# Performance work log

Measured on AMD Instinct MI355X. Metric: run time of the kernel, lower is better.

The kernel has to match this reference:

```python
import jax, jax.numpy as jnp
import numpy as np

B, H, S, D = 4, 16, 4096, 64

def setup_inputs() -> dict:
    key = jax.random.key(0)
    kq, kk, kv, km = jax.random.split(key, 4)
    Q = jax.random.normal(kq, (B, H, S, D), dtype=jnp.float32)
    K = jax.random.normal(kk, (B, H, S, D), dtype=jnp.float32)
    V = jax.random.normal(kv, (B, H, S, D), dtype=jnp.float32)
    mask = jax.random.randint(km, (B, S), 0, 2, dtype=jnp.int32)
    return {"Q": Q, "K": K, "V": V, "mask": mask}

def reference(Q, K, V, mask):
    Q = jax.nn.relu(Q)
    K = jax.nn.relu(K)
    # zero out masked-out key positions: mask [B,S] -> [B,1,S,1]
    m = mask.astype(bool)[:, None, :, None]
    K = jnp.where(m, K, jnp.zeros((), K.dtype))
    # attn_inter = K^T V : [B,H,D,D]
    attn_inter = jnp.einsum('bhsd,bhse->bhde', K, V)
    # attn_weights = Q @ attn_inter : [B,H,S,D]
    attn_weights = jnp.einsum('bhsd,bhde->bhse', Q, attn_inter)
    # norm = Q @ sum_s K : [B,H,S,1]
    k_sum = K.sum(axis=2)  # [B,H,D]
    norm = jnp.einsum('bhsd,bhd->bhs', Q, k_sum)[..., None]
    return attn_weights / norm
```

## Files before the change

### kernel.cpp

```cpp
#include <hip/hip_runtime.h>
#include <hip/hip_bf16.h>

#define SDIM 4096
#define DDIM 64
#define HN   16
#define BH   64
#define NC   16

typedef __attribute__((ext_vector_type(8))) short short8;
typedef __attribute__((ext_vector_type(4))) float f32x4;

static __device__ __forceinline__ short f2bfs(float f) {
    __hip_bfloat16 h = __float2bfloat16(f);
    return *reinterpret_cast<short*>(&h);
}

__global__ __launch_bounds__(256, 4) void k1_kv(
    const float* __restrict__ K, const float* __restrict__ V,
    const int* __restrict__ mask,
    float* __restrict__ KVp, float* __restrict__ ksump)
{
    __shared__ float kb[4096];
    const int tid = threadIdx.x;
    const int w = tid >> 6, l = tid & 63;
    const int a = l & 15, q = l >> 4;
    const int bh = blockIdx.x >> 4, ch = blockIdx.x & 15;
    const int b  = bh >> 4;
    const long base = (long)bh * SDIM * DDIM;
    const int s0 = ch * 256;

    f32x4 acc[4];
#pragma unroll
    for (int i = 0; i < 4; ++i) acc[i] = (f32x4){0.f, 0.f, 0.f, 0.f};
    float ksacc[4] = {0.f, 0.f, 0.f, 0.f};

    for (int st = 0; st < 8; ++st) {
        const int sb = st * 32;
        const float* kp = K + base + (long)(s0 + sb + q * 8) * DDIM + a;
        const float* vp = V + base + (long)(s0 + sb + q * 8) * DDIM + w * 16 + a;
        const int*   mp = mask + b * SDIM + s0 + sb + q * 8;

        float kf[4][8], vf[8];
        int   mi[8];
#pragma unroll
        for (int j = 0; j < 8; ++j) {
            mi[j] = mp[j];
#pragma unroll
            for (int dt = 0; dt < 4; ++dt)
                kf[dt][j] = kp[j * 64 + dt * 16];
            vf[j] = vp[j * 64];
        }

        short8 af[4], bf;
#pragma unroll
        for (int dt = 0; dt < 4; ++dt) {
            short8 ta;
#pragma unroll
            for (int j = 0; j < 8; ++j) {
                float x = fmaxf(kf[dt][j], 0.f);
                x = mi[j] ? x : 0.f;
                ksacc[dt] += x;
                ta[j] = f2bfs(x);
            }
            af[dt] = ta;
        }
#pragma unroll
        for (int j = 0; j < 8; ++j) bf[j] = f2bfs(vf[j]);

#pragma unroll
        for (int dt = 0; dt < 4; ++dt)
            acc[dt] = __builtin_amdgcn_mfma_f32_16x16x32_bf16(
                af[dt], bf, acc[dt], 0, 0, 0);
    }

#pragma unroll
    for (int dt = 0; dt < 4; ++dt) {
        ksacc[dt] += __shfl_xor(ksacc[dt], 16);
        ksacc[dt] += __shfl_xor(ksacc[dt], 32);
    }
    if (w == 0 && q == 0) {
#pragma unroll
        for (int dt = 0; dt < 4; ++dt)
            ksump[((long)bh * NC + ch) * 64 + dt * 16 + a] = ksacc[dt];
    }

    __syncthreads();
#pragma unroll
    for (int dt = 0; dt < 4; ++dt)
#pragma unroll
        for (int r = 0; r < 4; ++r) {
            const int d = dt * 16 + q * 4 + r;
            const int e = w * 16 + a;
            kb[d * 64 + (e ^ (((d >> 3) & 3) << 4))] = acc[dt][r];
        }
    __syncthreads();
    float* outp = KVp + ((long)bh * NC + ch) * 4096;
#pragma unroll
    for (int i = 0; i < 16; ++i) {
        const int idx = i * 256 + tid;
        const int d = idx >> 6, e = idx & 63;
        outp[idx] = kb[d * 64 + (e ^ (((d >> 3) & 3) << 4))];
    }
}

__global__ __launch_bounds__(256) void k2_reduce(
    const float* __restrict__ KVp, const float* __restrict__ ksump,
    float* __restrict__ KV, float* __restrict__ ksum)
{
    const int bh = blockIdx.x >> 2;
    const int qt = blockIdx.x & 3;
    const int tid = threadIdx.x;
#pragma unroll
    for (int i = 0; i < 4; ++i) {
        const int idx = qt * 1024 + i * 256 + tid;
        float v = 0.f;
#pragma unroll
        for (int c = 0; c < NC; ++c) v += KVp[((long)bh * NC + c) * 4096 + idx];
        KV[(long)bh * 4096 + idx] = v;
    }
    if (qt == 0 && tid < 64) {
        float v = 0.f;
#pragma unroll
        for (int c = 0; c < NC; ++c) v += ksump[((long)bh * NC + c) * 64 + tid];
        ksum[bh * 64 + tid] = v;
    }
}

__global__ __launch_bounds__(256, 4) void k3_out(
    const float* __restrict__ Q, const float* __restrict__ KVm,
    const float* __restrict__ ksum, float* __restrict__ out)
{
    __shared__ float cbuf[4][16 * 68];
    const int tid  = threadIdx.x;
    const int w    = tid >> 6;
    const int l    = tid & 63;
    const int r16  = l & 15;
    const int quad = l >> 4;
    const int bh    = blockIdx.x >> 4;
    const int strip = blockIdx.x & 15;

    const float* kvp = KVm + (long)bh * 4096;
    short8 bfrag[2][4];
#pragma unroll
    for (int kh = 0; kh < 2; ++kh)
#pragma unroll
        for (int n = 0; n < 4; ++n) {
            short8 tmp;
#pragma unroll
            for (int j = 0; j < 8; ++j)
                tmp[j] = f2bfs(kvp[(kh * 32 + quad * 8 + j) * 64 + n * 16 + r16]);
            bfrag[kh][n] = tmp;
        }
    float ksv[16];
#pragma unroll
    for (int j = 0; j < 8; ++j) {
        ksv[j]     = ksum[bh * 64 + quad * 8 + j];
        ksv[j + 8] = ksum[bh * 64 + 32 + quad * 8 + j];
    }

    const int rowbase = strip * 256 + w * 64;
    const float* qptr = Q + ((long)bh * SDIM + rowbase + r16) * DDIM + quad * 8;
    float* obase = out + ((long)bh * SDIM + rowbase) * DDIM;
    float* cw = &cbuf[w][0];

    f32x4 a0 = *(const f32x4*)(qptr);
    f32x4 a1 = *(const f32x4*)(qptr + 4);
    f32x4 a2 = *(const f32x4*)(qptr + 32);
    f32x4 a3 = *(const f32x4*)(qptr + 36);

    for (int t = 0; t < 4; ++t) {
        f32x4 b0 = a0, b1 = a1, b2 = a2, b3 = a3;
        if (t < 3) {
            const float* qn = qptr + (t + 1) * 16 * DDIM;
            b0 = *(const f32x4*)(qn);
            b1 = *(const f32x4*)(qn + 4);
            b2 = *(const f32x4*)(qn + 32);
            b3 = *(const f32x4*)(qn + 36);
        }
#pragma unroll
        for (int j = 0; j < 4; ++j) {
            a0[j] = fmaxf(a0[j], 0.f); a1[j] = fmaxf(a1[j], 0.f);
            a2[j] = fmaxf(a2[j], 0.f); a3[j] = fmaxf(a3[j], 0.f);
        }
        float p = 0.f;
#pragma unroll
        for (int j = 0; j < 4; ++j) {
            p = fmaf(a0[j], ksv[j],      p);
            p = fmaf(a1[j], ksv[4 + j],  p);
            p = fmaf(a2[j], ksv[8 + j],  p);
            p = fmaf(a3[j], ksv[12 + j], p);
        }
        p += __shfl_xor(p, 16);
        p += __shfl_xor(p, 32);
        const float inv = __builtin_amdgcn_rcpf(p);

        short8 af0, af1;
#pragma unroll
        for (int j = 0; j < 4; ++j) {
            af0[j]     = f2bfs(a0[j]);
            af0[4 + j] = f2bfs(a1[j]);
            af1[j]     = f2bfs(a2[j]);
            af1[4 + j] = f2bfs(a3[j]);
        }

        f32x4 acc[4];
#pragma unroll
        for (int n = 0; n < 4; ++n) {
            acc[n] = (f32x4){0.f, 0.f, 0.f, 0.f};
            acc[n] = __builtin_amdgcn_mfma_f32_16x16x32_bf16(af0, bfrag[0][n], acc[n], 0, 0, 0);
            acc[n] = __builtin_amdgcn_mfma_f32_16x16x32_bf16(af1, bfrag[1][n], acc[n], 0, 0, 0);
        }

        float invr[4];
#pragma unroll
        for (int r = 0; r < 4; ++r) invr[r] = __shfl(inv, quad * 4 + r);

#pragma unroll
        for (int n = 0; n < 4; ++n)
#pragma unroll
            for (int r = 0; r < 4; ++r)
                cw[(quad * 4 + r) * 68 + n * 16 + r16] = acc[n][r] * invr[r];

        float* ot = obase + (t * 16) * DDIM;
#pragma unroll
        for (int i = 0; i < 4; ++i) {
            f32x4 v = *(const f32x4*)(cw + (i * 4 + quad) * 68 + r16 * 4);
            *(f32x4*)(ot + (i * 4 + quad) * DDIM + r16 * 4) = v;
        }
        a0 = b0; a1 = b1; a2 = b2; a3 = b3;
    }
}

extern "C" void kernel_launch(void* const* d_in, const int* in_sizes, int n_in,
                              void* d_out, int out_size, void* d_ws, size_t ws_size,
                              hipStream_t stream)
{
    const float* Q    = (const float*)d_in[0];
    const float* K    = (const float*)d_in[1];
    const float* V    = (const float*)d_in[2];
    const int*   mask = (const int*)d_in[3];
    float* out = (float*)d_out;

    float* KVp   = out;
    float* ksump = KVp + (long)BH * NC * 4096;
    float* KV    = (float*)d_ws;
    float* ksum  = KV + (long)BH * 4096;

    hipLaunchKernelGGL(k1_kv, dim3(BH * NC), dim3(256), 0, stream,
                       K, V, mask, KVp, ksump);
    hipLaunchKernelGGL(k2_reduce, dim3(BH * 4), dim3(256), 0, stream,
                       KVp, ksump, KV, ksum);
    hipLaunchKernelGGL(k3_out, dim3(BH * 16), dim3(256), 0, stream,
                       Q, KV, ksum, out);
}
```

Before: 62.51 us.

## Stage K/V chunks through transposed bf16 LDS tiles with coalesced vector loads

The K^T V partial kernel now loads K and V with coalesced float4 row loads instead of strided scalar column loads. It converts them to bf16, packs row pairs via lane shuffles, and writes them into transposed, padded, double-buffered LDS tiles from which MFMA fragments are read. The next 64-row chunk is prefetched into registers while the current one is processed, and the column sums are reduced across waves through LDS. The aim is to cut the uncoalesced global-load cost of the first kernel, at the price of more LDS traffic, extra shuffles and a barrier per chunk.

```diff
diff --git a/kernel.cpp b/kernel.cpp
--- a/kernel.cpp
+++ b/kernel.cpp
@@ -10,89 +10,149 @@
 typedef __attribute__((ext_vector_type(8))) short short8;
 typedef __attribute__((ext_vector_type(4))) float f32x4;
 
+static __device__ __forceinline__ unsigned f2bfu(float f) {
+    __hip_bfloat16 h = __float2bfloat16(f);
+    return (unsigned)*reinterpret_cast<unsigned short*>(&h);
+}
 static __device__ __forceinline__ short f2bfs(float f) {
     __hip_bfloat16 h = __float2bfloat16(f);
     return *reinterpret_cast<short*>(&h);
 }
+
+#define KTPITCH 136
 
 __global__ __launch_bounds__(256, 4) void k1_kv(
     const float* __restrict__ K, const float* __restrict__ V,
     const int* __restrict__ mask,
     float* __restrict__ KVp, float* __restrict__ ksump)
 {
-    __shared__ float kb[4096];
+    __shared__ __align__(16) char smem[35840];
+    char* const KT0 = smem;
+    char* const VT0 = smem + 8704;
+    char* const KT1 = smem + 17408;
+    char* const VT1 = smem + 26112;
+    float* const kswork = (float*)(smem + 34816);
+
     const int tid = threadIdx.x;
     const int w = tid >> 6, l = tid & 63;
-    const int a = l & 15, q = l >> 4;
+    const int a = l & 15, quad = l >> 4;
     const int bh = blockIdx.x >> 4, ch = blockIdx.x & 15;
     const int b  = bh >> 4;
     const long base = (long)bh * SDIM * DDIM;
     const int s0 = ch * 256;
 
+    const int rb  = tid >> 4;
+    const int c4  = (tid & 15) << 2;
+    const int par = rb & 1;
+
     f32x4 acc[4];
 #pragma unroll
     for (int i = 0; i < 4; ++i) acc[i] = (f32x4){0.f, 0.f, 0.f, 0.f};
-    float ksacc[4] = {0.f, 0.f, 0.f, 0.f};
-
-    for (int st = 0; st < 8; ++st) {
-        const int sb = st * 32;
-        const float* kp = K + base + (long)(s0 + sb + q * 8) * DDIM + a;
-        const float* vp = V + base + (long)(s0 + sb + q * 8) * DDIM + w * 16 + a;
-        const int*   mp = mask + b * SDIM + s0 + sb + q * 8;
-
-        float kf[4][8], vf[8];
-        int   mi[8];
-#pragma unroll
-        for (int j = 0; j < 8; ++j) {
-            mi[j] = mp[j];
+    float ks4[4] = {0.f, 0.f, 0.f, 0.f};
+
+    f32x4 kr[4], vr[4];
+    float mr[4];
+#pragma unroll
+    for (int i = 0; i < 4; ++i) {
+        const int row = rb + 16 * i;
+        kr[i] = *(const f32x4*)(K + base + (long)(s0 + row) * DDIM + c4);
+        vr[i] = *(const f32x4*)(V + base + (long)(s0 + row) * DDIM + c4);
+        mr[i] = mask[b * SDIM + s0 + row] ? 1.f : 0.f;
+    }
+
+    for (int t = 0; t < 4; ++t) {
+        char* const KT = (t & 1) ? KT1 : KT0;
+        char* const VT = (t & 1) ? VT1 : VT0;
+
+#pragma unroll
+        for (int i = 0; i < 4; ++i) {
+            const int row = rb + 16 * i;
+            const int sp  = row >> 1;
+            float kq[4], vq[4];
+            kq[0] = fmaxf(kr[i].x, 0.f) * mr[i];
+            kq[1] = fmaxf(kr[i].y, 0.f) * mr[i];
+            kq[2] = fmaxf(kr[i].z, 0.f) * mr[i];
+            kq[3] = fmaxf(kr[i].w, 0.f) * mr[i];
+            vq[0] = vr[i].x; vq[1] = vr[i].y; vq[2] = vr[i].z; vq[3] = vr[i].w;
+#pragma unroll
+            for (int j = 0; j < 4; ++j) ks4[j] += kq[j];
+            unsigned ku[4], vu[4];
+#pragma unroll
+            for (int j = 0; j < 4; ++j) {
+                ku[j] = f2bfu(kq[j]);
+                vu[j] = f2bfu(vq[j]);
+            }
+            unsigned kp32[4], vp32[4];
+#pragma unroll
+            for (int j = 0; j < 4; ++j) {
+                const unsigned pk = (unsigned)__shfl_xor((int)ku[j], 16);
+                const unsigned pv = (unsigned)__shfl_xor((int)vu[j], 16);
+                kp32[j] = par ? (pk | (ku[j] << 16)) : (ku[j] | (pk << 16));
+                vp32[j] = par ? (pv | (vu[j] << 16)) : (vu[j] | (pv << 16));
+            }
+            const int j0 = par * 2;
+            *(unsigned*)(KT + (c4 + j0)     * KTPITCH + sp * 4) = kp32[j0];
+            *(unsigned*)(KT + (c4 + j0 + 1) * KTPITCH + sp * 4) = kp32[j0 + 1];
+            *(unsigned*)(VT + (c4 + j0)     * KTPITCH + sp * 4) = vp32[j0];
+            *(unsigned*)(VT + (c4 + j0 + 1) * KTPITCH + sp * 4) = vp32[j0 + 1];
+        }
+
+        if (t < 3) {
+            const int r0n = s0 + (t + 1) * 64;
+#pragma unroll
+            for (int i = 0; i < 4; ++i) {
+                const int row = rb + 16 * i;
+                kr[i] = *(const f32x4*)(K + base + (long)(r0n + row) * DDIM + c4);
+                vr[i] = *(const f32x4*)(V + base + (long)(r0n + row) * DDIM + c4);
+                mr[i] = mask[b * SDIM + r0n + row] ? 1.f : 0.f;
+            }
+        }
+
+        __syncthreads();
+
+#pragma unroll
+        for (int kh = 0; kh < 2; ++kh) {
+            const int sof = kh * 64 + quad * 16;
+            short8 af[4];
+#pragma unroll
+            for (int dt = 0; dt < 4; ++dt) {
+                const char* rp = KT + (dt * 16 + a) * KTPITCH + sof;
+                const uint2 lo = *(const uint2*)rp;
+                const uint2 hi = *(const uint2*)(rp + 8);
+                int4 ra; ra.x = lo.x; ra.y = lo.y; ra.z = hi.x; ra.w = hi.y;
+                af[dt] = *(short8*)&ra;
+            }
+            const char* vp = VT + (w * 16 + a) * KTPITCH + sof;
+            const uint2 vlo = *(const uint2*)vp;
+            const uint2 vhi = *(const uint2*)(vp + 8);
+            int4 rb4; rb4.x = vlo.x; rb4.y = vlo.y; rb4.z = vhi.x; rb4.w = vhi.y;
+            const short8 bf = *(short8*)&rb4;
 #pragma unroll
             for (int dt = 0; dt < 4; ++dt)
-                kf[dt][j] = kp[j * 64 + dt * 16];
-            vf[j] = vp[j * 64];
-        }
-
-        short8 af[4], bf;
-#pragma unroll
-        for (int dt = 0; dt < 4; ++dt) {
-            short8 ta;
-#pragma unroll
-            for (int j = 0; j < 8; ++j) {
-                float x = fmaxf(kf[dt][j], 0.f);
-                x = mi[j] ? x : 0.f;
-                ksacc[dt] += x;
-                ta[j] = f2bfs(x);
-            }
-            af[dt] = ta;
-        }
-#pragma unroll
-        for (int j = 0; j < 8; ++j) bf[j] = f2bfs(vf[j]);
-
-#pragma unroll
-        for (int dt = 0; dt < 4; ++dt)
-            acc[dt] = __builtin_amdgcn_mfma_f32_16x16x32_bf16(
-                af[dt], bf, acc[dt], 0, 0, 0);
-    }
-
-#pragma unroll
-    for (int dt = 0; dt < 4; ++dt) {
-        ksacc[dt] += __shfl_xor(ksacc[dt], 16);
-        ksacc[dt] += __shfl_xor(ksacc[dt], 32);
-    }
-    if (w == 0 && q == 0) {
-#pragma unroll
-        for (int dt = 0; dt < 4; ++dt)
-            ksump[((long)bh * NC + ch) * 64 + dt * 16 + a] = ksacc[dt];
-    }
-
+                acc[dt] = __builtin_amdgcn_mfma_f32_16x16x32_bf16(
+                    af[dt], bf, acc[dt], 0, 0, 0);
+        }
+    }
+
+#pragma unroll
+    for (int j = 0; j < 4; ++j) {
+        ks4[j] += __shfl_xor(ks4[j], 16);
+        ks4[j] += __shfl_xor(ks4[j], 32);
+    }
     __syncthreads();
+    float* const kb = (float*)smem;
 #pragma unroll
     for (int dt = 0; dt < 4; ++dt)
 #pragma unroll
         for (int r = 0; r < 4; ++r) {
-            const int d = dt * 16 + q * 4 + r;
+            const int d = dt * 16 + quad * 4 + r;
             const int e = w * 16 + a;
             kb[d * 64 + (e ^ (((d >> 3) & 3) << 4))] = acc[dt][r];
         }
+    if (l < 16) {
+#pragma unroll
+        for (int j = 0; j < 4; ++j) kswork[w * 64 + l * 4 + j] = ks4[j];
+    }
     __syncthreads();
     float* outp = KVp + ((long)bh * NC + ch) * 4096;
 #pragma unroll
@@ -101,6 +161,9 @@
         const int d = idx >> 6, e = idx & 63;
         outp[idx] = kb[d * 64 + (e ^ (((d >> 3) & 3) << 4))];
     }
+    if (tid < 64)
+        ksump[((long)bh * NC + ch) * 64 + tid] =
+            kswork[tid] + kswork[64 + tid] + kswork[128 + tid] + kswork[192 + tid];
 }
 
 __global__ __launch_bounds__(256) void k2_reduce(
```

New measurement: 67.64 us. +8.2%, slower.
